# Performance work log

Measured on AMD Instinct MI355X. Metric: run time of the kernel, lower is better.

Reference implementation:

```python
import jax, jax.numpy as jnp
import numpy as np
import math

N_HEADS = 32
N_KV_HEADS = 8
HEAD_DIM = 64
ROPE_BASE = 10000.0


def _rope_cos_sin(L, dtype):
    # inv_freq: [head_dim/2]
    inv_freq = 1.0 / (ROPE_BASE ** (jnp.arange(0, HEAD_DIM, 2, dtype=jnp.float32) / HEAD_DIM))
    t = jnp.arange(L, dtype=jnp.float32)
    freqs = jnp.outer(t, inv_freq)            # [L, head_dim/2]
    emb = jnp.concatenate([freqs, freqs], -1)  # [L, head_dim]
    return jnp.cos(emb).astype(dtype), jnp.sin(emb).astype(dtype)


def _rotate_half(x):
    x1, x2 = jnp.split(x, 2, axis=-1)
    return jnp.concatenate([-x2, x1], axis=-1)


def setup_inputs() -> dict:
    key = jax.random.key(0)
    ks = jax.random.split(key, 5)
    B, L, D = 2, 2048, 2048
    s = 0.02
    return {
        "x": jax.random.normal(ks[0], (B, L, D), jnp.float32),
        "Wq": jax.random.normal(ks[1], (D, N_HEADS * HEAD_DIM), jnp.float32) * s,
        "Wk": jax.random.normal(ks[2], (D, N_KV_HEADS * HEAD_DIM), jnp.float32) * s,
        "Wv": jax.random.normal(ks[3], (D, N_KV_HEADS * HEAD_DIM), jnp.float32) * s,
        "Wo": jax.random.normal(ks[4], (N_HEADS * HEAD_DIM, D), jnp.float32) * s,
    }


def reference(x, Wq, Wk, Wv, Wo):
    B, L, D = x.shape
    G = N_HEADS // N_KV_HEADS
    # QKV projections -> [B, H, L, hd]
    q = (x @ Wq).reshape(B, L, N_HEADS, HEAD_DIM).transpose(0, 2, 1, 3)
    k = (x @ Wk).reshape(B, L, N_KV_HEADS, HEAD_DIM).transpose(0, 2, 1, 3)
    v = (x @ Wv).reshape(B, L, N_KV_HEADS, HEAD_DIM).transpose(0, 2, 1, 3)
    # RoPE
    cos, sin = _rope_cos_sin(L, x.dtype)  # [L, hd]
    cos = cos[None, None]
    sin = sin[None, None]
    q = q * cos + _rotate_half(q) * sin
    k = k * cos + _rotate_half(k) * sin
    # GQA expand kv heads (repeat_interleave along head dim)
    k = jnp.repeat(k, G, axis=1)
    v = jnp.repeat(v, G, axis=1)
    # Causal SDPA
    scale = 1.0 / math.sqrt(HEAD_DIM)
    scores = jnp.einsum('bhqd,bhkd->bhqk', q, k) * scale  # [B,H,L,L]
    causal = jnp.tril(jnp.ones((L, L), bool))
    scores = jnp.where(causal[None, None], scores, jnp.finfo(scores.dtype).min)
    probs = jax.nn.softmax(scores, axis=-1)
    out = jnp.einsum('bhqk,bhkd->bhqd', probs, v)  # [B,H,L,hd]
    out = out.transpose(0, 2, 1, 3).reshape(B, L, N_HEADS * HEAD_DIM)
    return out @ Wo
```

## Files before the change

kernel.cpp:

```cpp
#include <hip/hip_runtime.h>
#include <hip/hip_bf16.h>
#include <stdint.h>

typedef __bf16 bf16_t;
typedef bf16_t bf16x2 __attribute__((ext_vector_type(2)));
typedef bf16_t bf16x4 __attribute__((ext_vector_type(4)));
typedef bf16_t bf16x8 __attribute__((ext_vector_type(8)));
typedef float f32x4 __attribute__((ext_vector_type(4)));
typedef float f32x16 __attribute__((ext_vector_type(16)));

#define NH 32
#define NKV 8
#define HD 64
#define LSEQ 2048
#define DMODEL 2048
#define BATCH 2

#define QSCALE 0.18033688011112042f
#define FIXED_M 12.0f

__device__ __forceinline__ void gl_lds16(const void* g, void* l) {
  __builtin_amdgcn_global_load_lds(
      (__attribute__((address_space(1))) char*)(uintptr_t)g,
      (__attribute__((address_space(3))) char*)(uintptr_t)l, 16, 0, 0);
}

__device__ __forceinline__ unsigned pack2(float a, float b) {
  bf16x2 t;
  t[0] = (bf16_t)a;
  t[1] = (bf16_t)b;
  return __builtin_bit_cast(unsigned, t);
}

__device__ __forceinline__ void transpose_tile32(
    const float* __restrict__ W, bf16_t* __restrict__ WT, int K, int N,
    int bi, float* tile ) {
  const int n32 = N >> 5;
  const int nb = (bi & (n32 - 1)) * 32, kb = (bi / n32) * 32;
  const int tx = threadIdx.x & 31, ty = threadIdx.x >> 5;
#pragma unroll
  for (int i = 0; i < 32; i += 8)
    tile[(ty + i) * 33 + tx] = W[(size_t)(kb + ty + i) * N + nb + tx];
  __syncthreads();
#pragma unroll
  for (int i = 0; i < 32; i += 8)
    WT[(size_t)(nb + ty + i) * K + kb + tx] = (bf16_t)tile[tx * 33 + ty + i];
}

__global__ __launch_bounds__(256) void prep_all(
    const float* __restrict__ x, const float* __restrict__ Wq,
    const float* __restrict__ Wk, const float* __restrict__ Wv,
    const float* __restrict__ Wo, bf16_t* __restrict__ xb,
    bf16_t* __restrict__ wqkvT, bf16_t* __restrict__ wot,
    float* __restrict__ cosT, float* __restrict__ sinT) {
  __shared__ float tile[32 * 33];
  const int bx = blockIdx.x;
  if (bx < 8192) {
    const int i = bx * 256 + threadIdx.x;
    const float4 v = ((const float4*)x)[i];
    bf16x4 o;
    o[0] = (bf16_t)v.x; o[1] = (bf16_t)v.y; o[2] = (bf16_t)v.z; o[3] = (bf16_t)v.w;
    ((bf16x4*)xb)[i] = o;
  } else if (bx < 12288) {
    transpose_tile32(Wq, wqkvT, 2048, 2048, bx - 8192, tile);
  } else if (bx < 13312) {
    transpose_tile32(Wk, wqkvT + (size_t)2048 * 2048, 2048, 512, bx - 12288, tile);
  } else if (bx < 14336) {
    transpose_tile32(Wv, wqkvT + (size_t)2560 * 2048, 2048, 512, bx - 13312, tile);
  } else if (bx < 18432) {
    transpose_tile32(Wo, wot, 2048, 2048, bx - 14336, tile);
  } else {
    const int t = (bx - 18432) * 256 + threadIdx.x;
    const int l = t >> 5, i = t & 31;
    const float inv = powf(10000.0f, -(float)i / 32.0f);
    const float ang = (float)l * inv;
    float s, c;
    sincosf(ang, &s, &c);
    cosT[t] = c;
    sinT[t] = s;
  }
}

__global__ __launch_bounds__(256) void rope_scatter(
    const bf16_t* __restrict__ QKVf, const float* __restrict__ cosT,
    const float* __restrict__ sinT, bf16_t* __restrict__ Qh,
    bf16_t* __restrict__ Kh, bf16_t* __restrict__ VTh) {
  const int bx = blockIdx.x;
  if (bx < 2560) {
    const int hh = bx >> 6;
    const int rg = bx & 63;
    const bool isQ = hh < 32;
    const int d = threadIdx.x & 31, rs = threadIdx.x >> 5;
    const float sc = isQ ? QSCALE : 1.0f;
#pragma unroll
    for (int rr = 0; rr < 8; ++rr) {
      const int row = rg * 64 + rr * 8 + rs;
      const int ls = row & (LSEQ - 1), bb = row >> 11;
      const float a = (float)QKVf[(size_t)row * 3072 + hh * 64 + d];
      const float b2 = (float)QKVf[(size_t)row * 3072 + hh * 64 + 32 + d];
      const float c = cosT[ls * 32 + d], s = sinT[ls * 32 + d];
      bf16_t* dst = isQ
          ? Qh + (((size_t)bb * NH + hh) * LSEQ + ls) * HD + d
          : Kh + (((size_t)bb * NKV + (hh - 32)) * LSEQ + ls) * HD + d;
      dst[0] = (bf16_t)((a * c - b2 * s) * sc);
      dst[32] = (bf16_t)((b2 * c + a * s) * sc);
    }
  } else {
    __shared__ bf16_t vt[64][68];
    const int i2 = bx - 2560;
    const int vh = i2 >> 6, rg = i2 & 63;
    const int c64 = threadIdx.x & 63, q4 = threadIdx.x >> 6;
#pragma unroll
    for (int rr = 0; rr < 16; ++rr) {
      const int lrow = rr * 4 + q4;
      vt[lrow][c64] =
          QKVf[(size_t)(rg * 64 + lrow) * 3072 + 2560 + vh * 64 + c64];
    }
    __syncthreads();
    const int row0 = rg * 64;
    const int bb = row0 >> 11, ls0 = row0 & (LSEQ - 1);
#pragma unroll
    for (int rr = 0; rr < 16; ++rr) {
      const int dd = rr * 4 + q4;
      VTh[(((size_t)bb * NKV + vh) * HD + dd) * LSEQ + ls0 + c64] =
          vt[c64][dd];
    }
  }
}

template <int EPI, int NREP>
__global__ __launch_bounds__(512, 1) void gemm256(
    const bf16_t* __restrict__ A, const bf16_t* __restrict__ BT,
    void* __restrict__ Cp, int M, int N, int K, int nx) {
  __shared__ bf16_t Al[2][4 * 4096];
  __shared__ bf16_t Bl[2][NREP * 4096];
  const int tid = threadIdx.x, lane = tid & 63, w = tid >> 6;
  const int wm = w >> 2, wn = w & 3;
  const int r15 = lane & 15, g = lane >> 4;
  const int nwg = (int)gridDim.x;
  const int sid = ((int)blockIdx.x & 7) * (nwg >> 3) + ((int)blockIdx.x >> 3);
  const int m0 = (sid / nx) * 256, n0 = (sid % nx) * (NREP * 64);

  f32x4 acc[8][NREP] = {};

  const int NT = K >> 6;
  const int NI = NT >> 1;

  auto stage_q = [&](bf16_t* dst, const bf16_t* src, int row0, int kt) {
    const int r = tid >> 3;
    const int sc = (((tid & 7) ^ (r & 7)) << 3);
    gl_lds16(src + (size_t)(row0 + r) * K + (kt << 6) + sc, dst + tid * 8);
  };
  auto stage_step = [&](int d, int kt, int s) {
    kt = kt < NT ? kt : NT - 1;
    if (s == 0) { stage_q(&Bl[d][0], BT, n0, kt); stage_q(&Bl[d][4096], BT, n0 + 64, kt); }
    else if (s == 1) { stage_q(&Al[d][0], A, m0, kt); stage_q(&Al[d][8192], A, m0 + 128, kt); }
    else if (s == 2) { stage_q(&Al[d][4096], A, m0 + 64, kt); stage_q(&Al[d][12288], A, m0 + 192, kt); }
  };
  auto lda = [&](int d, int mi, int kk) -> bf16x8 {
    const int ar = (wm << 7) + (mi << 4) + r15;
    return *(const bf16x8*)((const char*)&Al[d][(ar >> 6) << 12] +
                            (ar & 63) * 128 + ((((kk << 2) + g) ^ (ar & 7)) << 4));
  };
  auto ldb = [&](int d, int ni, int kk) -> bf16x8 {
    const int br = wn * (NREP << 4) + (ni << 4) + r15;
    return *(const bf16x8*)((const char*)&Bl[d][(br >> 6) << 12] +
                            (br & 63) * 128 + ((((kk << 2) + g) ^ (br & 7)) << 4));
  };

  stage_step(0, 0, 0);
  stage_step(0, 0, 1);
  stage_step(0, 0, 2);
  stage_step(0, 0, 3);

  for (int i = 0; i < NI; ++i) {
#pragma unroll
    for (int hf = 0; hf < 2; ++hf) {
      const int dC = hf;
      const int dS = hf ^ 1;
      const int ktS = (i << 1) + 1 + hf;
      bf16x8 bf0[NREP][2];
#pragma unroll
      for (int q = 0; q < 4; ++q) {
        stage_step(dS, ktS, q);
        if (q == 0) asm volatile("s_waitcnt vmcnt(4)" ::: "memory");
        if (q == 2) asm volatile("s_waitcnt vmcnt(6)" ::: "memory");
        __builtin_amdgcn_s_barrier();
        asm volatile("" ::: "memory");
        if (q == 0) {
#pragma unroll
          for (int ni = 0; ni < NREP; ++ni)
#pragma unroll
            for (int kk = 0; kk < 2; ++kk) bf0[ni][kk] = ldb(dC, ni, kk);
        }
        bf16x8 af[2][2];
#pragma unroll
        for (int t2 = 0; t2 < 2; ++t2)
#pragma unroll
          for (int kk = 0; kk < 2; ++kk) af[t2][kk] = lda(dC, 2 * q + t2, kk);
        __builtin_amdgcn_s_setprio(1);
#pragma unroll
        for (int t2 = 0; t2 < 2; ++t2)
#pragma unroll
          for (int ni = 0; ni < NREP; ++ni)
#pragma unroll
            for (int kk = 0; kk < 2; ++kk)
              acc[2 * q + t2][ni] = __builtin_amdgcn_mfma_f32_16x16x32_bf16(
                  af[t2][kk], bf0[ni][kk], acc[2 * q + t2][ni], 0, 0, 0);
        __builtin_amdgcn_s_setprio(0);
        asm volatile("" ::: "memory");
        __builtin_amdgcn_s_barrier();
      }
    }
  }
  asm volatile("s_waitcnt vmcnt(0)" ::: "memory");

  if constexpr (EPI == 0) {
    float* Cf = (float*)Cp;
#pragma unroll
    for (int mi = 0; mi < 8; ++mi) {
      const int row = m0 + wm * 128 + mi * 16 + g * 4;
#pragma unroll
      for (int ni = 0; ni < NREP; ++ni) {
        const int col = n0 + wn * (NREP * 16) + ni * 16 + r15;
#pragma unroll
        for (int r = 0; r < 4; ++r)
          Cf[(size_t)(row + r) * N + col] = acc[mi][ni][r];
      }
    }
  } else {
    bf16_t* Cb = (bf16_t*)Cp;
#pragma unroll
    for (int mi = 0; mi < 8; ++mi) {
      const int row = m0 + wm * 128 + mi * 16 + g * 4;
#pragma unroll
      for (int ni = 0; ni < NREP; ++ni) {
        const int col = n0 + wn * (NREP * 16) + ni * 16 + r15;
#pragma unroll
        for (int r = 0; r < 4; ++r)
          Cb[(size_t)(row + r) * N + col] = (bf16_t)acc[mi][ni][r];
      }
    }
  }
}

__global__ __launch_bounds__(512, 4) void attn_fwd(
    const bf16_t* __restrict__ Q, const bf16_t* __restrict__ Kh,
    const bf16_t* __restrict__ VTh, bf16_t* __restrict__ AO) {
  __shared__ bf16_t Kl[2][64 * 64];
  __shared__ bf16_t Vl[2][64 * 64];
  const int tid = threadIdx.x, lane = tid & 63, w = tid >> 6;
  const int col = lane & 31, hi = lane >> 5;
  const int hk = (int)blockIdx.x & 7, b = (int)blockIdx.x >> 3;
  const int a = (int)blockIdx.y & 15, k = (int)blockIdx.y >> 4;
  const int qt = k ? 31 - a : a;
  const int h = hk * 4 + (w & 3);
  const int qoff = (w >> 2) * 32;

  const bf16_t* Qb =
      Q + (((size_t)b * NH + h) * LSEQ + (size_t)qt * 64 + qoff) * HD;
  const bf16_t* Kb = Kh + ((size_t)b * NKV + hk) * LSEQ * HD;
  const bf16_t* Vb = VTh + ((size_t)b * NKV + hk) * HD * LSEQ;

  const int nt = qt + 1;

  auto stage = [&](int buf, int kt) {
    const int row = tid >> 3, cc = tid & 7;
    const int scol = (cc ^ (row & 7)) * 16;
    gl_lds16((const char*)Kb + (size_t)(kt * 64 + row) * 128 + scol,
             (char*)&Kl[buf][0] + tid * 16);
    gl_lds16((const char*)Vb + (size_t)row * 4096 + (size_t)kt * 128 + scol,
             (char*)&Vl[buf][0] + tid * 16);
  };

  bf16x8 qf[4];
#pragma unroll
  for (int kc = 0; kc < 4; ++kc)
    qf[kc] = *(const bf16x8*)&Qb[(size_t)col * HD + kc * 16 + hi * 8];

  f32x16 o[2] = {};
  float lsum = 0.f;

  int cur = 0;
  stage(cur, 0);
  __syncthreads();
  for (int kt = 0; kt < nt; ++kt) {
    if (kt + 1 < nt) stage(cur ^ 1, kt + 1);
    const bool diag = (kt == nt - 1);
    const char* Kcur = (const char*)&Kl[cur][0];
    const char* Vcur = (const char*)&Vl[cur][0];

    f32x16 sfrag[2] = {};
#pragma unroll
    for (int kvs = 0; kvs < 2; ++kvs) {
      if (diag && kvs * 32 > 31 + qoff) {
#pragma unroll
        for (int r = 0; r < 16; ++r) sfrag[kvs][r] = -1e30f;
        continue;
      }
      bf16x8 ak[4];
#pragma unroll
      for (int kc = 0; kc < 4; ++kc) {
        const int row = kvs * 32 + col;
        const int slot = ((kc * 2 + hi) ^ (row & 7)) * 16;
        ak[kc] = *(const bf16x8*)(Kcur + row * 128 + slot);
      }
#pragma unroll
      for (int kc = 0; kc < 4; ++kc)
        sfrag[kvs] = __builtin_amdgcn_mfma_f32_32x32x16_bf16(
            ak[kc], qf[kc], sfrag[kvs], 0, 0, 0);
    }

    if (diag) {
#pragma unroll
      for (int kvs = 0; kvs < 2; ++kvs)
#pragma unroll
        for (int r = 0; r < 16; ++r) {
          const int kvl = kvs * 32 + (r & 3) + 8 * (r >> 2) + 4 * hi;
          if (kvl > col + qoff) sfrag[kvs][r] = -1e30f;
        }
    }

    bf16x8 pf[4];
#pragma unroll
    for (int kvs = 0; kvs < 2; ++kvs)
#pragma unroll
      for (int c1 = 0; c1 < 2; ++c1) {
        float pv[8];
#pragma unroll
        for (int j = 0; j < 8; ++j) {
          pv[j] = __builtin_amdgcn_exp2f(sfrag[kvs][c1 * 8 + j] - FIXED_M);
          lsum += pv[j];
        }
        const unsigned a01 = pack2(pv[0], pv[1]), a23 = pack2(pv[2], pv[3]);
        const unsigned b01 = pack2(pv[4], pv[5]), b23 = pack2(pv[6], pv[7]);
        const unsigned s01 = __shfl_xor(hi ? a01 : b01, 32);
        const unsigned s23 = __shfl_xor(hi ? a23 : b23, 32);
        union { unsigned u[4]; bf16x8 v; } t;
        t.u[0] = hi ? s01 : a01;
        t.u[1] = hi ? s23 : a23;
        t.u[2] = hi ? b01 : s01;
        t.u[3] = hi ? b23 : s23;
        pf[kvs * 2 + c1] = t.v;
      }

#pragma unroll
    for (int ds = 0; ds < 2; ++ds) {
      bf16x8 av[4];
#pragma unroll
      for (int kc2 = 0; kc2 < 4; ++kc2) {
        const int row = ds * 32 + col;
        const int slot = ((kc2 * 2 + hi) ^ (row & 7)) * 16;
        av[kc2] = *(const bf16x8*)(Vcur + row * 128 + slot);
      }
#pragma unroll
      for (int kc2 = 0; kc2 < 4; ++kc2) {
        if (diag && kc2 * 16 > 31 + qoff) continue;
        o[ds] = __builtin_amdgcn_mfma_f32_32x32x16_bf16(
            av[kc2], pf[kc2], o[ds], 0, 0, 0);
      }
    }

    __syncthreads();
    cur ^= 1;
  }

  lsum += __shfl_xor(lsum, 32);
  const float inv = 1.0f / lsum;
  const int q = qt * 64 + qoff + col;
#pragma unroll
  for (int ds = 0; ds < 2; ++ds)
#pragma unroll
    for (int g4 = 0; g4 < 4; ++g4) {
      bf16x4 o4;
#pragma unroll
      for (int j = 0; j < 4; ++j) o4[j] = (bf16_t)(o[ds][g4 * 4 + j] * inv);
      const int d = ds * 32 + 8 * g4 + 4 * hi;
      *(bf16x4*)&AO[((size_t)b * LSEQ + q) * DMODEL + h * HD + d] = o4;
    }
}


extern "C" void kernel_launch(void* const* d_in, const int* in_sizes, int n_in,
                              void* d_out, int out_size, void* d_ws, size_t ws_size,
                              hipStream_t stream) {
  const float* x = (const float*)d_in[0];
  const float* Wq = (const float*)d_in[1];
  const float* Wk = (const float*)d_in[2];
  const float* Wv = (const float*)d_in[3];
  const float* Wo = (const float*)d_in[4];
  char* ws = (char*)d_ws;
  size_t off = 0;
  auto alloc = [&](size_t bytes) {
    char* p = ws + off;
    off += (bytes + 255) & ~(size_t)255;
    return p;
  };
  bf16_t* xb = (bf16_t*)alloc((size_t)BATCH * LSEQ * DMODEL * 2);
  bf16_t* wqkvT = (bf16_t*)alloc((size_t)3072 * DMODEL * 2);
  bf16_t* wot = (bf16_t*)alloc((size_t)DMODEL * DMODEL * 2);
  float* cosT = (float*)alloc((size_t)LSEQ * 32 * 4);
  float* sinT = (float*)alloc((size_t)LSEQ * 32 * 4);
  bf16_t* QKVf = (bf16_t*)alloc((size_t)BATCH * LSEQ * 3072 * 2);
  bf16_t* Qh = (bf16_t*)alloc((size_t)BATCH * NH * LSEQ * HD * 2);
  bf16_t* Kh = (bf16_t*)alloc((size_t)BATCH * NKV * LSEQ * HD * 2);
  bf16_t* VTh = (bf16_t*)alloc((size_t)BATCH * NKV * HD * LSEQ * 2);
  bf16_t* AO = (bf16_t*)alloc((size_t)BATCH * LSEQ * NH * HD * 2);
  (void)ws_size; (void)in_sizes; (void)n_in; (void)out_size;

  const int M = BATCH * LSEQ;

  prep_all<<<18688, 256, 0, stream>>>(x, Wq, Wk, Wv, Wo, xb, wqkvT, wot,
                                      cosT, sinT);

  gemm256<1, 2><<<384, 512, 0, stream>>>(
      xb, wqkvT, QKVf, M, 3072, 2048, 24);

  rope_scatter<<<3072, 256, 0, stream>>>(QKVf, cosT, sinT, Qh, Kh, VTh);

  attn_fwd<<<dim3(16, 32), 512, 0, stream>>>(Qh, Kh, VTh, AO);

  gemm256<0, 2><<<256, 512, 0, stream>>>(
      AO, wot, (float*)d_out, M, 2048, 2048, 16);
}
```

Baseline: 181.6 us.

## Fuse Q RoPE into attention load and split QKV GEMM into Q and KV

The Q projection is written straight to a row-major buffer, and the attention kernel now loads Q rows from it, applying RoPE and the softmax scale in registers. This removes Q from the scatter kernel and avoids writing and re-reading a head-major Q copy. The single QKV GEMM becomes two launches, a 256-block Q GEMM and a 128-block KV GEMM, so the KV GEMM may fill the GPU less well and adds a launch. Q loads in attention are now strided by 2048 elements rather than contiguous per head.

```diff
diff --git a/kernel.cpp b/kernel.cpp
--- a/kernel.cpp
+++ b/kernel.cpp
@@ -81,40 +81,36 @@
   }
 }
 
-__global__ __launch_bounds__(256) void rope_scatter(
-    const bf16_t* __restrict__ QKVf, const float* __restrict__ cosT,
-    const float* __restrict__ sinT, bf16_t* __restrict__ Qh,
-    bf16_t* __restrict__ Kh, bf16_t* __restrict__ VTh) {
+__global__ __launch_bounds__(256) void kv_scatter(
+    const bf16_t* __restrict__ KVf, const float* __restrict__ cosT,
+    const float* __restrict__ sinT, bf16_t* __restrict__ Kh,
+    bf16_t* __restrict__ VTh) {
   const int bx = blockIdx.x;
-  if (bx < 2560) {
+  if (bx < 512) {
     const int hh = bx >> 6;
     const int rg = bx & 63;
-    const bool isQ = hh < 32;
     const int d = threadIdx.x & 31, rs = threadIdx.x >> 5;
-    const float sc = isQ ? QSCALE : 1.0f;
 #pragma unroll
     for (int rr = 0; rr < 8; ++rr) {
       const int row = rg * 64 + rr * 8 + rs;
       const int ls = row & (LSEQ - 1), bb = row >> 11;
-      const float a = (float)QKVf[(size_t)row * 3072 + hh * 64 + d];
-      const float b2 = (float)QKVf[(size_t)row * 3072 + hh * 64 + 32 + d];
+      const float a = (float)KVf[(size_t)row * 1024 + hh * 64 + d];
+      const float b2 = (float)KVf[(size_t)row * 1024 + hh * 64 + 32 + d];
       const float c = cosT[ls * 32 + d], s = sinT[ls * 32 + d];
-      bf16_t* dst = isQ
-          ? Qh + (((size_t)bb * NH + hh) * LSEQ + ls) * HD + d
-          : Kh + (((size_t)bb * NKV + (hh - 32)) * LSEQ + ls) * HD + d;
-      dst[0] = (bf16_t)((a * c - b2 * s) * sc);
-      dst[32] = (bf16_t)((b2 * c + a * s) * sc);
+      bf16_t* dst = Kh + (((size_t)bb * NKV + hh) * LSEQ + ls) * HD + d;
+      dst[0] = (bf16_t)(a * c - b2 * s);
+      dst[32] = (bf16_t)(b2 * c + a * s);
     }
   } else {
     __shared__ bf16_t vt[64][68];
-    const int i2 = bx - 2560;
+    const int i2 = bx - 512;
     const int vh = i2 >> 6, rg = i2 & 63;
     const int c64 = threadIdx.x & 63, q4 = threadIdx.x >> 6;
 #pragma unroll
     for (int rr = 0; rr < 16; ++rr) {
       const int lrow = rr * 4 + q4;
       vt[lrow][c64] =
-          QKVf[(size_t)(rg * 64 + lrow) * 3072 + 2560 + vh * 64 + c64];
+          KVf[(size_t)(rg * 64 + lrow) * 1024 + 512 + vh * 64 + c64];
     }
     __syncthreads();
     const int row0 = rg * 64;
@@ -245,8 +241,9 @@
 }
 
 __global__ __launch_bounds__(512, 4) void attn_fwd(
-    const bf16_t* __restrict__ Q, const bf16_t* __restrict__ Kh,
-    const bf16_t* __restrict__ VTh, bf16_t* __restrict__ AO) {
+    const bf16_t* __restrict__ QKVq, const bf16_t* __restrict__ Kh,
+    const bf16_t* __restrict__ VTh, const float* __restrict__ cosT,
+    const float* __restrict__ sinT, bf16_t* __restrict__ AO) {
   __shared__ bf16_t Kl[2][64 * 64];
   __shared__ bf16_t Vl[2][64 * 64];
   const int tid = threadIdx.x, lane = tid & 63, w = tid >> 6;
@@ -258,7 +255,7 @@
   const int qoff = (w >> 2) * 32;
 
   const bf16_t* Qb =
-      Q + (((size_t)b * NH + h) * LSEQ + (size_t)qt * 64 + qoff) * HD;
+      QKVq + ((size_t)(b * LSEQ + qt * 64 + qoff)) * 2048 + h * HD;
   const bf16_t* Kb = Kh + ((size_t)b * NKV + hk) * LSEQ * HD;
   const bf16_t* Vb = VTh + ((size_t)b * NKV + hk) * HD * LSEQ;
 
@@ -273,10 +270,23 @@
              (char*)&Vl[buf][0] + tid * 16);
   };
 
+  bf16x8 qraw[4];
+#pragma unroll
+  for (int kc = 0; kc < 4; ++kc)
+    qraw[kc] = *(const bf16x8*)&Qb[(size_t)col * 2048 + kc * 16 + hi * 8];
+  const int lsq = qt * 64 + qoff + col;
   bf16x8 qf[4];
 #pragma unroll
-  for (int kc = 0; kc < 4; ++kc)
-    qf[kc] = *(const bf16x8*)&Qb[(size_t)col * HD + kc * 16 + hi * 8];
+  for (int kc2 = 0; kc2 < 2; ++kc2)
+#pragma unroll
+    for (int j = 0; j < 8; ++j) {
+      const int p = kc2 * 16 + hi * 8 + j;
+      const float c = cosT[lsq * 32 + p], s = sinT[lsq * 32 + p];
+      const float lo = (float)qraw[kc2][j];
+      const float hv = (float)qraw[kc2 + 2][j];
+      qf[kc2][j] = (bf16_t)((lo * c - hv * s) * QSCALE);
+      qf[kc2 + 2][j] = (bf16_t)((hv * c + lo * s) * QSCALE);
+    }
 
   f32x16 o[2] = {};
   float lsum = 0.f;
@@ -401,8 +411,8 @@
   bf16_t* wot = (bf16_t*)alloc((size_t)DMODEL * DMODEL * 2);
   float* cosT = (float*)alloc((size_t)LSEQ * 32 * 4);
   float* sinT = (float*)alloc((size_t)LSEQ * 32 * 4);
-  bf16_t* QKVf = (bf16_t*)alloc((size_t)BATCH * LSEQ * 3072 * 2);
-  bf16_t* Qh = (bf16_t*)alloc((size_t)BATCH * NH * LSEQ * HD * 2);
+  bf16_t* QKVq = (bf16_t*)alloc((size_t)BATCH * LSEQ * 2048 * 2);
+  bf16_t* KVf = (bf16_t*)alloc((size_t)BATCH * LSEQ * 1024 * 2);
   bf16_t* Kh = (bf16_t*)alloc((size_t)BATCH * NKV * LSEQ * HD * 2);
   bf16_t* VTh = (bf16_t*)alloc((size_t)BATCH * NKV * HD * LSEQ * 2);
   bf16_t* AO = (bf16_t*)alloc((size_t)BATCH * LSEQ * NH * HD * 2);
@@ -413,12 +423,15 @@
   prep_all<<<18688, 256, 0, stream>>>(x, Wq, Wk, Wv, Wo, xb, wqkvT, wot,
                                       cosT, sinT);
 
-  gemm256<1, 2><<<384, 512, 0, stream>>>(
-      xb, wqkvT, QKVf, M, 3072, 2048, 24);
-
-  rope_scatter<<<3072, 256, 0, stream>>>(QKVf, cosT, sinT, Qh, Kh, VTh);
-
-  attn_fwd<<<dim3(16, 32), 512, 0, stream>>>(Qh, Kh, VTh, AO);
+  gemm256<1, 2><<<256, 512, 0, stream>>>(
+      xb, wqkvT, QKVq, M, 2048, 2048, 16);
+
+  gemm256<1, 2><<<128, 512, 0, stream>>>(
+      xb, wqkvT + (size_t)2048 * 2048, KVf, M, 1024, 2048, 8);
+
+  kv_scatter<<<1024, 256, 0, stream>>>(KVf, cosT, sinT, Kh, VTh);
+
+  attn_fwd<<<dim3(16, 32), 512, 0, stream>>>(QKVq, Kh, VTh, cosT, sinT, AO);
 
   gemm256<0, 2><<<256, 512, 0, stream>>>(
       AO, wot, (float*)d_out, M, 2048, 2048, 16);
```

After: 185.1 us. Within noise of the previous version (+1.9%).
